# Kernel optimization log

Measured on AMD Instinct MI355X. Metric: run time of the kernel, lower is better.

## Reference

```python
import jax, jax.numpy as jnp
import numpy as np

B, N, C, H = 4, 2048, 1024, 16
D = C // H  # head dim


def setup_inputs() -> dict:
    key = jax.random.key(0)
    ks = jax.random.split(key, 9)
    s = 1.0 / np.sqrt(C)
    inp = {"x": jax.random.normal(ks[0], (B, N, C), dtype=jnp.float32)}
    names = ["wq", "wk", "wv", "wo"]
    for i, n in enumerate(names):
        inp[n] = jax.random.uniform(ks[1 + 2 * i], (C, C), dtype=jnp.float32, minval=-s, maxval=s)
        inp["b" + n[1]] = jax.random.uniform(ks[2 + 2 * i], (C,), dtype=jnp.float32, minval=-s, maxval=s)
    return inp


def reference(x, wq, bq, wk, bk, wv, bv, wo, bo):
    b, n, c = x.shape
    # projections; weights stored as (in, out) so y = x @ w + b
    def split_heads(y):
        return y.reshape(b, n, H, D).transpose(0, 2, 1, 3)  # (B,H,N,D)

    q = split_heads(x @ wq + bq)
    k = split_heads(x @ wk + bk)
    v = split_heads(x @ wv + bv)
    scores = jnp.einsum("bhnd,bhmd->bhnm", q, k) / np.sqrt(D).astype(x.dtype)
    attn = jax.nn.softmax(scores, axis=-1)
    ctx = jnp.einsum("bhnm,bhmd->bhnd", attn, v)
    out = ctx.transpose(0, 2, 1, 3).reshape(b, n, c)
    return out @ wo + bo
```

## Files before the change

### kernel.cpp

```cpp
#include <hip/hip_runtime.h>
#include <hip/hip_bf16.h>
#include <hip/hip_fp16.h>

#define SEQ 2048
#define NH  16
#define DH  64
#define CH  1024
#define BATCH 4
#define BH (BATCH*NH)
#define MTOK (BATCH*SEQ)

typedef unsigned short u16;
typedef _Float16 h8 __attribute__((ext_vector_type(8)));
typedef float f4 __attribute__((ext_vector_type(4)));
typedef float f16x __attribute__((ext_vector_type(16)));

#define AS1(p) ((const __attribute__((address_space(1))) unsigned int*)(p))
#define AS3(p) ((__attribute__((address_space(3))) unsigned int*)(p))

__device__ __forceinline__ u16 f2h(float f) {
  _Float16 h = (_Float16)f;
  return __builtin_bit_cast(unsigned short, h);
}

__device__ __forceinline__ unsigned pk_rne(float a, float b) {
  return (unsigned)f2h(a) | ((unsigned)f2h(b) << 16);
}

__device__ __forceinline__ float ex2(float x) { return __builtin_amdgcn_exp2f(x); }

__device__ __forceinline__ float max16_3(const f16x& v) {
  float a = fmaxf(fmaxf(v[0], v[1]), v[2]);
  float b = fmaxf(fmaxf(v[3], v[4]), v[5]);
  float c = fmaxf(fmaxf(v[6], v[7]), v[8]);
  float d = fmaxf(fmaxf(v[9], v[10]), v[11]);
  float e = fmaxf(fmaxf(v[12], v[13]), v[14]);
  float f = fmaxf(fmaxf(a, b), v[15]);
  return fmaxf(fmaxf(fmaxf(c, d), e), f);
}

__global__ __launch_bounds__(256) void k_convert_x(const float* __restrict__ x,
                                                   u16* __restrict__ xh) {
  int idx = (blockIdx.x * 256 + threadIdx.x) * 8;
  float4 a = *(const float4*)(x + idx);
  float4 b = *(const float4*)(x + idx + 4);
  uint4 o;
  o.x = (unsigned)f2h(a.x) | ((unsigned)f2h(a.y) << 16);
  o.y = (unsigned)f2h(a.z) | ((unsigned)f2h(a.w) << 16);
  o.z = (unsigned)f2h(b.x) | ((unsigned)f2h(b.y) << 16);
  o.w = (unsigned)f2h(b.z) | ((unsigned)f2h(b.w) << 16);
  *(uint4*)(xh + idx) = o;
}

__global__ __launch_bounds__(256) void k_transpose_w(const float* __restrict__ w0,
                                                     const float* __restrict__ w1,
                                                     const float* __restrict__ w2,
                                                     const float* __restrict__ w3,
                                                     u16* __restrict__ dst_all) {
  int mat = blockIdx.z;
  const float* src = (mat == 0) ? w0 : (mat == 1) ? w1 : (mat == 2) ? w2 : w3;
  u16* dst = dst_all + (size_t)mat * (CH * CH);
  __shared__ float t[64][65];
  int n0 = blockIdx.x * 64, k0 = blockIdx.y * 64;
#pragma unroll
  for (int i = 0; i < 16; ++i) {
    int idx = threadIdx.x + i * 256;
    int r = idx >> 6, c = idx & 63;
    t[r][c] = src[(size_t)(k0 + r) * CH + n0 + c];
  }
  __syncthreads();
#pragma unroll
  for (int i = 0; i < 16; ++i) {
    int idx = threadIdx.x + i * 256;
    int r = idx >> 6, c = idx & 63;
    dst[(size_t)(n0 + r) * CH + k0 + c] = f2h(t[c][r]);
  }
}

__global__ __launch_bounds__(256) void k_transpose_v(const u16* __restrict__ v,
                                                     u16* __restrict__ vt) {
  int n0 = blockIdx.x * 64;
  int bh = blockIdx.y;
  __shared__ u16 t[64][68];
  const u16* src = v + (size_t)bh * SEQ * DH + (size_t)n0 * DH;
#pragma unroll
  for (int i = 0; i < 4; ++i) {
    int g = threadIdx.x + i * 256;
    int r = g >> 4, c4 = (g & 15) * 4;
    *(ushort4*)&t[r][c4] = *(const ushort4*)(src + (size_t)r * DH + c4);
  }
  __syncthreads();
  u16* dst = vt + (size_t)bh * DH * SEQ + n0;
#pragma unroll
  for (int i = 0; i < 4; ++i) {
    int g = threadIdx.x + i * 256;
    int d = g >> 4, k4 = (g & 15) * 4;
    ushort4 o;
    o.x = t[k4 + 0][d]; o.y = t[k4 + 1][d]; o.z = t[k4 + 2][d]; o.w = t[k4 + 3][d];
    *(ushort4*)(dst + (size_t)d * SEQ + k4) = o;
  }
}

__global__ __launch_bounds__(256) void k_gemm_qkv(
    const u16* __restrict__ xh, const u16* __restrict__ wt,
    const float* __restrict__ bq, const float* __restrict__ bk,
    const float* __restrict__ bv,
    u16* __restrict__ qo, u16* __restrict__ ko, u16* __restrict__ vo) {
  const int tid = threadIdx.x;
  const int lane = tid & 63;
  const int wv = tid >> 6;
  const int wr = wv >> 1, wc = wv & 1;
  const int l16 = lane & 15, g = lane >> 4;
  const int tm = blockIdx.x;
  const int tn = blockIdx.y;
  const int mat = tn >> 3;
  const int nbase = (tn & 7) * 128;
  const u16* wb = wt + (size_t)mat * (CH * CH);

  __shared__ u16 As[128 * 32];
  __shared__ u16 Bs[128 * 32];

  f4 zero = {0.f, 0.f, 0.f, 0.f};
  f4 acc[4][4];
#pragma unroll
  for (int m = 0; m < 4; ++m)
#pragma unroll
    for (int n = 0; n < 4; ++n) acc[m][n] = zero;

  for (int k0 = 0; k0 < CH; k0 += 32) {
#pragma unroll
    for (int j = 0; j < 2; ++j) {
      int rbase = wv * 32 + j * 16;
      int row = rbase + (lane >> 2);
      int blk = (lane & 3) ^ ((row >> 1) & 3);
      const u16* ga = xh + (size_t)(tm * 128 + row) * CH + k0 + blk * 8;
      __builtin_amdgcn_global_load_lds(AS1(ga), AS3(&As[rbase * 32]), 16, 0, 0);
      const u16* gb = wb + (size_t)(nbase + row) * CH + k0 + blk * 8;
      __builtin_amdgcn_global_load_lds(AS1(gb), AS3(&Bs[rbase * 32]), 16, 0, 0);
    }
    __syncthreads();

    h8 af[4], bf[4];
#pragma unroll
    for (int i = 0; i < 4; ++i) {
      int arow = wr * 64 + i * 16 + l16;
      af[i] = *(const h8*)&As[arow * 32 + ((g ^ ((arow >> 1) & 3)) * 8)];
      int brow = wc * 64 + i * 16 + l16;
      bf[i] = *(const h8*)&Bs[brow * 32 + ((g ^ ((brow >> 1) & 3)) * 8)];
    }
#pragma unroll
    for (int m = 0; m < 4; ++m)
#pragma unroll
      for (int n = 0; n < 4; ++n)
        acc[m][n] = __builtin_amdgcn_mfma_f32_16x16x32_f16(af[m], bf[n], acc[m][n], 0, 0, 0);
    __syncthreads();
  }

  const float* bias = (mat == 0) ? bq : (mat == 1) ? bk : bv;
  u16* outp = (mat == 0) ? qo : (mat == 1) ? ko : vo;
  const float qscale = (mat == 0) ? 0.125f * 1.44269504f : 1.0f;
#pragma unroll
  for (int n = 0; n < 4; ++n) {
    int col = nbase + wc * 64 + n * 16 + l16;
    float bcol = bias[col];
    int h_ = col >> 6, d_ = col & 63;
#pragma unroll
    for (int m = 0; m < 4; ++m) {
#pragma unroll
      for (int r = 0; r < 4; ++r) {
        int t = tm * 128 + wr * 64 + m * 16 + g * 4 + r;
        int b_ = t >> 11, nseq = t & 2047;
        float val = (acc[m][n][r] + bcol) * qscale;
        outp[(((size_t)(b_ * NH + h_) * SEQ) + nseq) * DH + d_] = f2h(val);
      }
    }
  }
}

__global__ __launch_bounds__(256, 4) void k_attn(const u16* __restrict__ q,
                                                 const u16* __restrict__ k,
                                                 const u16* __restrict__ vt,
                                                 u16* __restrict__ ctx) {
  const int qb0 = blockIdx.x;
  const int bh = blockIdx.y;
  const int tid = threadIdx.x;
  const int lane = tid & 63;
  const int w = tid >> 6;
  const int l31 = lane & 31;
  const int hi = lane >> 5;

  __shared__ u16 Ks[2][32 * 128];
  __shared__ u16 Vs[2][32 * 128];

  const u16* kbase = k + (size_t)bh * SEQ * DH;
  const u16* vbase = vt + (size_t)bh * DH * SEQ;
  const u16* qbase = q + (size_t)bh * SEQ * DH;
  const int q0 = qb0 * 128 + w * 32;

  h8 qf[4];
#pragma unroll
  for (int ds = 0; ds < 4; ++ds)
    qf[ds] = *(const h8*)(qbase + (size_t)(q0 + l31) * DH + 16 * ds + 8 * hi);

  int koff[2][4];
  int voff[2][2][2];
#pragma unroll
  for (int h = 0; h < 2; ++h) {
#pragma unroll
    for (int ds = 0; ds < 4; ++ds) {
      int slot = 8 * h + 2 * ds + hi;
      koff[h][ds] = l31 * 128 + ((slot ^ (l31 & 15)) * 8);
    }
#pragma unroll
    for (int db = 0; db < 2; ++db)
#pragma unroll
      for (int ks = 0; ks < 2; ++ks) {
        int slot = 8 * db + 4 * h + 2 * ks + hi;
        voff[h][db][ks] = l31 * 128 + ((slot ^ (l31 & 15)) * 8);
      }
  }

  const u16* gk[2];
  const u16* gv[2];
#pragma unroll
  for (int c = 0; c < 2; ++c) {
    int r2 = w * 8 + c * 4 + (lane >> 4);
    int S = (lane & 15) ^ (r2 & 15);
    gk[c] = kbase + (size_t)(r2 + 32 * (S >> 3)) * DH + (S & 7) * 8;
    gv[c] = vbase + (size_t)(r2 + 32 * (S >> 3)) * SEQ + (S & 7) * 8;
  }

  f16x accq[2];
  accq[0] = {}; accq[1] = {};
  float m0 = 0.f, l0 = 0.f;

  auto STAGE = [&](int bi) {
#pragma unroll
    for (int c = 0; c < 2; ++c) {
      __builtin_amdgcn_global_load_lds(AS1(gk[c]), AS3(&Ks[bi][(w * 8 + c * 4) * 128]), 16, 0, 0);
      __builtin_amdgcn_global_load_lds(AS1(gv[c]), AS3(&Vs[bi][(w * 8 + c * 4) * 128]), 16, 0, 0);
      gk[c] += 64 * DH;
      gv[c] += 64;
    }
  };

  auto pack8 = [&](const float* p, int ks) -> h8 {
    unsigned a0 = pk_rne(p[8 * ks + 0], p[8 * ks + 1]);
    unsigned c0 = pk_rne(p[8 * ks + 2], p[8 * ks + 3]);
    unsigned b0 = pk_rne(p[8 * ks + 4], p[8 * ks + 5]);
    unsigned d0 = pk_rne(p[8 * ks + 6], p[8 * ks + 7]);
    unsigned s1 = __shfl_xor(hi ? a0 : b0, 32, 64);
    unsigned s2 = __shfl_xor(hi ? c0 : d0, 32, 64);
    uint4 wds;
    wds.x = hi ? s1 : a0;
    wds.y = hi ? s2 : c0;
    wds.z = hi ? b0 : s1;
    wds.w = hi ? d0 : s2;
    return __builtin_bit_cast(h8, wds);
  };

  auto SUBSTEP = [&](const u16* Kb, const u16* Vb, int h) {
    f16x s = {};
#pragma unroll
    for (int ds = 0; ds < 4; ++ds) {
      h8 kf = *(const h8*)(Kb + koff[h][ds]);
      s = __builtin_amdgcn_mfma_f32_32x32x16_f16(kf, qf[ds], s, 0, 0, 0);
    }
    float tmx = max16_3(s);
    tmx = fmaxf(tmx, __shfl_xor(tmx, 32, 64));
    if (!__all(tmx <= m0 + 8.f)) {
      float mn = fmaxf(m0, tmx);
      float sc = ex2(m0 - mn);
      m0 = mn; l0 *= sc;
#pragma unroll
      for (int r = 0; r < 16; ++r) {
        int src = (lane & 32) + ((r & 3) + 8 * (r >> 2) + 4 * hi);
        float scr = __shfl(sc, src, 64);
        accq[0][r] *= scr; accq[1][r] *= scr;
      }
    }
    float p[16];
    float rs = 0.f;
#pragma unroll
    for (int r = 0; r < 16; ++r) { p[r] = ex2(s[r] - m0); rs += p[r]; }
    l0 += rs + __shfl_xor(rs, 32, 64);

    h8 pa0 = pack8(p, 0);
    h8 pa1 = pack8(p, 1);
#pragma unroll
    for (int db = 0; db < 2; ++db) {
      h8 vf0 = *(const h8*)(Vb + voff[h][db][0]);
      accq[db] = __builtin_amdgcn_mfma_f32_32x32x16_f16(pa0, vf0, accq[db], 0, 0, 0);
      h8 vf1 = *(const h8*)(Vb + voff[h][db][1]);
      accq[db] = __builtin_amdgcn_mfma_f32_32x32x16_f16(pa1, vf1, accq[db], 0, 0, 0);
    }
  };

  STAGE(0);
  for (int kt = 0; kt < SEQ / 64; kt += 2) {
    __syncthreads();
    STAGE(1);
    SUBSTEP(&Ks[0][0], &Vs[0][0], 0);
    SUBSTEP(&Ks[0][0], &Vs[0][0], 1);
    __syncthreads();
    if (kt + 2 < SEQ / 64) STAGE(0);
    SUBSTEP(&Ks[1][0], &Vs[1][0], 0);
    SUBSTEP(&Ks[1][0], &Vs[1][0], 1);
  }

  float inv0 = 1.0f / l0;
  int b_ = bh >> 4, h_ = bh & 15;
#pragma unroll
  for (int r = 0; r < 16; ++r) {
    int row = (r & 3) + 8 * (r >> 2) + 4 * hi;
    int src = (lane & 32) + row;
    float i0 = __shfl(inv0, src, 64);
#pragma unroll
    for (int db = 0; db < 2; ++db) {
      ctx[((size_t)(b_ * SEQ + q0 + row)) * CH + h_ * 64 + 32 * db + l31] =
          f2h(accq[db][r] * i0);
    }
  }
}

__global__ __launch_bounds__(256) void k_gemm_out(const u16* __restrict__ ctxb,
                                                  const u16* __restrict__ wot,
                                                  const float* __restrict__ bo,
                                                  float* __restrict__ out) {
  const int tid = threadIdx.x;
  const int lane = tid & 63;
  const int wv = tid >> 6;
  const int wr = wv >> 1, wc = wv & 1;
  const int l16 = lane & 15, g = lane >> 4;
  const int tm = blockIdx.x;
  const int nbase = blockIdx.y * 128;

  __shared__ u16 As[128 * 32];
  __shared__ u16 Bs[128 * 32];

  f4 zero = {0.f, 0.f, 0.f, 0.f};
  f4 acc[4][4];
#pragma unroll
  for (int m = 0; m < 4; ++m)
#pragma unroll
    for (int n = 0; n < 4; ++n) acc[m][n] = zero;

  for (int k0 = 0; k0 < CH; k0 += 32) {
#pragma unroll
    for (int j = 0; j < 2; ++j) {
      int rbase = wv * 32 + j * 16;
      int row = rbase + (lane >> 2);
      int blk = (lane & 3) ^ ((row >> 1) & 3);
      const u16* ga = ctxb + (size_t)(tm * 128 + row) * CH + k0 + blk * 8;
      __builtin_amdgcn_global_load_lds(AS1(ga), AS3(&As[rbase * 32]), 16, 0, 0);
      const u16* gb = wot + (size_t)(nbase + row) * CH + k0 + blk * 8;
      __builtin_amdgcn_global_load_lds(AS1(gb), AS3(&Bs[rbase * 32]), 16, 0, 0);
    }
    __syncthreads();

    h8 af[4], bf[4];
#pragma unroll
    for (int i = 0; i < 4; ++i) {
      int arow = wr * 64 + i * 16 + l16;
      af[i] = *(const h8*)&As[arow * 32 + ((g ^ ((arow >> 1) & 3)) * 8)];
      int brow = wc * 64 + i * 16 + l16;
      bf[i] = *(const h8*)&Bs[brow * 32 + ((g ^ ((brow >> 1) & 3)) * 8)];
    }
#pragma unroll
    for (int m = 0; m < 4; ++m)
#pragma unroll
      for (int n = 0; n < 4; ++n)
        acc[m][n] = __builtin_amdgcn_mfma_f32_16x16x32_f16(af[m], bf[n], acc[m][n], 0, 0, 0);
    __syncthreads();
  }

#pragma unroll
  for (int n = 0; n < 4; ++n) {
    int col = nbase + wc * 64 + n * 16 + l16;
    float bcol = bo[col];
#pragma unroll
    for (int m = 0; m < 4; ++m) {
#pragma unroll
      for (int r = 0; r < 4; ++r) {
        int t = tm * 128 + wr * 64 + m * 16 + g * 4 + r;
        out[(size_t)t * CH + col] = acc[m][n][r] + bcol;
      }
    }
  }
}

extern "C" void kernel_launch(void* const* d_in, const int* in_sizes, int n_in,
                              void* d_out, int out_size, void* d_ws, size_t ws_size,
                              hipStream_t stream) {
  (void)in_sizes; (void)n_in; (void)out_size; (void)ws_size;
  const float* x  = (const float*)d_in[0];
  const float* wq = (const float*)d_in[1];
  const float* bq = (const float*)d_in[2];
  const float* wk = (const float*)d_in[3];
  const float* bk = (const float*)d_in[4];
  const float* wv = (const float*)d_in[5];
  const float* bv = (const float*)d_in[6];
  const float* wo = (const float*)d_in[7];
  const float* bo = (const float*)d_in[8];
  float* out = (float*)d_out;

  char* ws = (char*)d_ws;
  u16* xh   = (u16*)(ws);
  u16* wt   = (u16*)(ws + 16777216);
  u16* qbuf = (u16*)(ws + 25165824);
  u16* kbuf = (u16*)(ws + 41943040);
  u16* vbuf = (u16*)(ws + 58720256);
  u16* ctxb = (u16*)(ws + 75497472);
  u16* wot  = wt + 3 * CH * CH;
  u16* vtb  = xh;

  k_convert_x<<<dim3(4096), dim3(256), 0, stream>>>(x, xh);
  k_transpose_w<<<dim3(16, 16, 4), dim3(256), 0, stream>>>(wq, wk, wv, wo, wt);
  k_gemm_qkv<<<dim3(64, 24), dim3(256), 0, stream>>>(xh, wt, bq, bk, bv, qbuf, kbuf, vbuf);
  k_transpose_v<<<dim3(32, 64), dim3(256), 0, stream>>>(vbuf, vtb);
  k_attn<<<dim3(16, 64), dim3(256), 0, stream>>>(qbuf, kbuf, vtb, ctxb);
  k_gemm_out<<<dim3(64, 8), dim3(256), 0, stream>>>(ctxb, wot, bo, out);
}
```

Measured before the change: 221.9 us.

## Fuse V transpose into QKV GEMM epilogue and trim softmax shuffles

The QKV projection now writes V directly in transposed (B,H,D,N) layout with 4-wide stores, so the separate transpose kernel and its extra read/write pass are dropped. In attention, P packing uses the hardware round-toward-zero pack conversion instead of two scalar round-to-nearest conversions. The cross-half shuffle of the row max now runs only when a rescale is needed, and the row-sum shuffle is deferred to one reduction after the loop. Risks are slightly different rounding of P and the rescale test now using a per-half max.

Measured after the change: 239.3 us. 7.9% more time.

```diff
diff --git a/kernel.cpp b/kernel.cpp
--- a/kernel.cpp
+++ b/kernel.cpp
@@ -23,8 +23,9 @@
   return __builtin_bit_cast(unsigned short, h);
 }
 
-__device__ __forceinline__ unsigned pk_rne(float a, float b) {
-  return (unsigned)f2h(a) | ((unsigned)f2h(b) << 16);
+__device__ __forceinline__ unsigned cvtpk(float a, float b) {
+  auto t = __builtin_amdgcn_cvt_pkrtz(a, b);
+  return __builtin_bit_cast(unsigned, t);
 }
 
 __device__ __forceinline__ float ex2(float x) { return __builtin_amdgcn_exp2f(x); }
@@ -77,35 +78,11 @@
   }
 }
 
-__global__ __launch_bounds__(256) void k_transpose_v(const u16* __restrict__ v,
-                                                     u16* __restrict__ vt) {
-  int n0 = blockIdx.x * 64;
-  int bh = blockIdx.y;
-  __shared__ u16 t[64][68];
-  const u16* src = v + (size_t)bh * SEQ * DH + (size_t)n0 * DH;
-#pragma unroll
-  for (int i = 0; i < 4; ++i) {
-    int g = threadIdx.x + i * 256;
-    int r = g >> 4, c4 = (g & 15) * 4;
-    *(ushort4*)&t[r][c4] = *(const ushort4*)(src + (size_t)r * DH + c4);
-  }
-  __syncthreads();
-  u16* dst = vt + (size_t)bh * DH * SEQ + n0;
-#pragma unroll
-  for (int i = 0; i < 4; ++i) {
-    int g = threadIdx.x + i * 256;
-    int d = g >> 4, k4 = (g & 15) * 4;
-    ushort4 o;
-    o.x = t[k4 + 0][d]; o.y = t[k4 + 1][d]; o.z = t[k4 + 2][d]; o.w = t[k4 + 3][d];
-    *(ushort4*)(dst + (size_t)d * SEQ + k4) = o;
-  }
-}
-
 __global__ __launch_bounds__(256) void k_gemm_qkv(
     const u16* __restrict__ xh, const u16* __restrict__ wt,
     const float* __restrict__ bq, const float* __restrict__ bk,
     const float* __restrict__ bv,
-    u16* __restrict__ qo, u16* __restrict__ ko, u16* __restrict__ vo) {
+    u16* __restrict__ qo, u16* __restrict__ ko, u16* __restrict__ vo_t) {
   const int tid = threadIdx.x;
   const int lane = tid & 63;
   const int wv = tid >> 6;
@@ -157,21 +134,41 @@
   }
 
   const float* bias = (mat == 0) ? bq : (mat == 1) ? bk : bv;
-  u16* outp = (mat == 0) ? qo : (mat == 1) ? ko : vo;
-  const float qscale = (mat == 0) ? 0.125f * 1.44269504f : 1.0f;
-#pragma unroll
-  for (int n = 0; n < 4; ++n) {
-    int col = nbase + wc * 64 + n * 16 + l16;
-    float bcol = bias[col];
-    int h_ = col >> 6, d_ = col & 63;
-#pragma unroll
-    for (int m = 0; m < 4; ++m) {
-#pragma unroll
-      for (int r = 0; r < 4; ++r) {
-        int t = tm * 128 + wr * 64 + m * 16 + g * 4 + r;
-        int b_ = t >> 11, nseq = t & 2047;
-        float val = (acc[m][n][r] + bcol) * qscale;
-        outp[(((size_t)(b_ * NH + h_) * SEQ) + nseq) * DH + d_] = f2h(val);
+  if (mat == 2) {
+#pragma unroll
+    for (int n = 0; n < 4; ++n) {
+      int col = nbase + wc * 64 + n * 16 + l16;
+      float bcol = bias[col];
+      int h_ = col >> 6, d_ = col & 63;
+#pragma unroll
+      for (int m = 0; m < 4; ++m) {
+        int t0 = tm * 128 + wr * 64 + m * 16 + g * 4;
+        int b_ = t0 >> 11, nseq0 = t0 & 2047;
+        ushort4 o;
+        o.x = f2h(acc[m][n][0] + bcol);
+        o.y = f2h(acc[m][n][1] + bcol);
+        o.z = f2h(acc[m][n][2] + bcol);
+        o.w = f2h(acc[m][n][3] + bcol);
+        *(ushort4*)&vo_t[(((size_t)(b_ * NH + h_) * DH) + d_) * SEQ + nseq0] = o;
+      }
+    }
+  } else {
+    u16* outp = (mat == 0) ? qo : ko;
+    const float qscale = (mat == 0) ? 0.125f * 1.44269504f : 1.0f;
+#pragma unroll
+    for (int n = 0; n < 4; ++n) {
+      int col = nbase + wc * 64 + n * 16 + l16;
+      float bcol = bias[col];
+      int h_ = col >> 6, d_ = col & 63;
+#pragma unroll
+      for (int m = 0; m < 4; ++m) {
+#pragma unroll
+        for (int r = 0; r < 4; ++r) {
+          int t = tm * 128 + wr * 64 + m * 16 + g * 4 + r;
+          int b_ = t >> 11, nseq = t & 2047;
+          float val = (acc[m][n][r] + bcol) * qscale;
+          outp[(((size_t)(b_ * NH + h_) * SEQ) + nseq) * DH + d_] = f2h(val);
+        }
       }
     }
   }
@@ -245,10 +242,10 @@
   };
 
   auto pack8 = [&](const float* p, int ks) -> h8 {
-    unsigned a0 = pk_rne(p[8 * ks + 0], p[8 * ks + 1]);
-    unsigned c0 = pk_rne(p[8 * ks + 2], p[8 * ks + 3]);
-    unsigned b0 = pk_rne(p[8 * ks + 4], p[8 * ks + 5]);
-    unsigned d0 = pk_rne(p[8 * ks + 6], p[8 * ks + 7]);
+    unsigned a0 = cvtpk(p[8 * ks + 0], p[8 * ks + 1]);
+    unsigned c0 = cvtpk(p[8 * ks + 2], p[8 * ks + 3]);
+    unsigned b0 = cvtpk(p[8 * ks + 4], p[8 * ks + 5]);
+    unsigned d0 = cvtpk(p[8 * ks + 6], p[8 * ks + 7]);
     unsigned s1 = __shfl_xor(hi ? a0 : b0, 32, 64);
     unsigned s2 = __shfl_xor(hi ? c0 : d0, 32, 64);
     uint4 wds;
@@ -267,9 +264,9 @@
       s = __builtin_amdgcn_mfma_f32_32x32x16_f16(kf, qf[ds], s, 0, 0, 0);
     }
     float tmx = max16_3(s);
-    tmx = fmaxf(tmx, __shfl_xor(tmx, 32, 64));
     if (!__all(tmx <= m0 + 8.f)) {
-      float mn = fmaxf(m0, tmx);
+      float tm2 = fmaxf(tmx, __shfl_xor(tmx, 32, 64));
+      float mn = fmaxf(m0, tm2);
       float sc = ex2(m0 - mn);
       m0 = mn; l0 *= sc;
 #pragma unroll
@@ -283,7 +280,7 @@
     float rs = 0.f;
 #pragma unroll
     for (int r = 0; r < 16; ++r) { p[r] = ex2(s[r] - m0); rs += p[r]; }
-    l0 += rs + __shfl_xor(rs, 32, 64);
+    l0 += rs;
 
     h8 pa0 = pack8(p, 0);
     h8 pa1 = pack8(p, 1);
@@ -308,6 +305,7 @@
     SUBSTEP(&Ks[1][0], &Vs[1][0], 1);
   }
 
+  l0 += __shfl_xor(l0, 32, 64);
   float inv0 = 1.0f / l0;
   int b_ = bh >> 4, h_ = bh & 15;
 #pragma unroll
@@ -412,12 +410,10 @@
   u16* vbuf = (u16*)(ws + 58720256);
   u16* ctxb = (u16*)(ws + 75497472);
   u16* wot  = wt + 3 * CH * CH;
-  u16* vtb  = xh;
 
   k_convert_x<<<dim3(4096), dim3(256), 0, stream>>>(x, xh);
   k_transpose_w<<<dim3(16, 16, 4), dim3(256), 0, stream>>>(wq, wk, wv, wo, wt);
   k_gemm_qkv<<<dim3(64, 24), dim3(256), 0, stream>>>(xh, wt, bq, bk, bv, qbuf, kbuf, vbuf);
-  k_transpose_v<<<dim3(32, 64), dim3(256), 0, stream>>>(vbuf, vtb);
-  k_attn<<<dim3(16, 64), dim3(256), 0, stream>>>(qbuf, kbuf, vtb, ctxb);
+  k_attn<<<dim3(16, 64), dim3(256), 0, stream>>>(qbuf, kbuf, vbuf, ctxb);
   k_gemm_out<<<dim3(64, 8), dim3(256), 0, stream>>>(ctxb, wot, bo, out);
 }
```
